# Kernel optimization log

Measured on AMD Instinct MI355X. Metric: run time of the kernel, lower is better.

Reference implementation:

```python
import jax, jax.numpy as jnp
import numpy as np

DT = 1.0
SPIKE_THRESHOLD = 30.0


def setup_inputs() -> dict:
    key = jax.random.key(0)
    kx, = jax.random.split(key, 1)
    x = jax.random.normal(kx, (16, 64, 1024, 32), dtype=jnp.float32)
    # scalar learnable parameters (Izhikevich model constants)
    a = jnp.float32(0.02)
    b = jnp.float32(0.2)
    c = jnp.float32(-65.0)
    d = jnp.float32(8.0)
    return {"x": x, "a": a, "b": b, "c": c, "d": d}


def reference(x, a, b, c, d):
    # x: [B, C, N, T]. Initial membrane potential v and recovery u are zeros.
    B, C, N, T = x.shape
    v0 = jnp.zeros((B, C, N), dtype=x.dtype)
    u0 = jnp.zeros((B, C, N), dtype=x.dtype)
    xs = jnp.moveaxis(x, -1, 0)  # [T, B, C, N] time-major for scan

    def step(carry, x_t):
        v, u = carry
        dv = 0.04 * v * v + 5.0 * v + 140.0 - u + x_t
        v = v + DT * dv
        du = a * (b * v - u)
        u = u + DT * du
        spike = (v >= SPIKE_THRESHOLD).astype(x_t.dtype)
        v = v * (1.0 - spike) + c * spike
        u = u + d * spike
        return (v, u), spike

    (_, _), spikes = jax.lax.scan(step, (v0, u0), xs)
    return jnp.moveaxis(spikes, 0, -1)  # [B, C, N, T]
```

## Files before the change

kernel.cpp:

```cpp
#include <hip/hip_runtime.h>


#define T_STEPS 32

__global__ __launch_bounds__(256) void izhikevich_kernel(
    const float* __restrict__ x,
    const float* __restrict__ pa,
    const float* __restrict__ pb,
    const float* __restrict__ pc,
    const float* __restrict__ pd,
    float* __restrict__ out,
    int n_neurons)
{
#pragma clang fp contract(off)
    const int n = blockIdx.x * blockDim.x + threadIdx.x;
    if (n >= n_neurons) return;

    const float a = pa[0];
    const float b = pb[0];
    const float c = pc[0];
    const float d = pd[0];

    const float4* __restrict__ xp =
        reinterpret_cast<const float4*>(x + (size_t)n * T_STEPS);
    float4* __restrict__ op =
        reinterpret_cast<float4*>(out + (size_t)n * T_STEPS);

    float4 xs[8];
#pragma unroll
    for (int k = 0; k < 8; ++k) xs[k] = xp[k];
    const float* xf = reinterpret_cast<const float*>(xs);

    float v = 0.0f;
    float u = 0.0f;

#pragma unroll
    for (int k = 0; k < 8; ++k) {
        float4 sp;
        float* sf = reinterpret_cast<float*>(&sp);
#pragma unroll
        for (int j = 0; j < 4; ++j) {
            const float xt = xf[k * 4 + j];
            const float t1 = (0.04f * v) * v;
            const float t2 = 5.0f * v;
            const float dv = (((t1 + t2) + 140.0f) - u) + xt;
            v = v + dv;
            const float du = a * ((b * v) - u);
            u = u + du;
            const float spike = (v >= 30.0f) ? 1.0f : 0.0f;
            const float oms = 1.0f - spike;
            v = (v * oms) + (c * spike);
            u = u + (d * spike);
            sf[j] = spike;
        }
        op[k] = sp;
    }
}

extern "C" void kernel_launch(void* const* d_in, const int* in_sizes, int n_in,
                              void* d_out, int out_size, void* d_ws, size_t ws_size,
                              hipStream_t stream) {
    const float* x  = (const float*)d_in[0];
    const float* pa = (const float*)d_in[1];
    const float* pb = (const float*)d_in[2];
    const float* pc = (const float*)d_in[3];
    const float* pd = (const float*)d_in[4];
    float* out = (float*)d_out;

    const int n_neurons = in_sizes[0] / T_STEPS;
    const int block = 256;
    const int grid = (n_neurons + block - 1) / block;

    izhikevich_kernel<<<grid, block, 0, stream>>>(x, pa, pb, pc, pd, out,
                                                  n_neurons);
}
```

Measured before the change: 265.1 us.

## Coalesce global loads and stores by transposing through padded shared memory

Each block now loads its contiguous input tile with fully coalesced float4 accesses, transposes it through a padded LDS buffer so each thread reads its own neuron's time series, and stages spikes back through LDS for coalesced stores. This replaces per-thread strided 128-byte accesses. It adds two barriers and LDS traffic, and drops the tail bounds check, so it assumes the neuron count is a multiple of the block size.

```diff
diff --git a/kernel.cpp b/kernel.cpp
--- a/kernel.cpp
+++ b/kernel.cpp
@@ -2,58 +2,72 @@
 
 
 #define T_STEPS 32
+#define TPB 256
+#define ROW 33
 
-__global__ __launch_bounds__(256) void izhikevich_kernel(
+__global__ __launch_bounds__(TPB) void izhikevich_kernel(
     const float* __restrict__ x,
     const float* __restrict__ pa,
     const float* __restrict__ pb,
     const float* __restrict__ pc,
     const float* __restrict__ pd,
-    float* __restrict__ out,
-    int n_neurons)
+    float* __restrict__ out)
 {
 #pragma clang fp contract(off)
-    const int n = blockIdx.x * blockDim.x + threadIdx.x;
-    if (n >= n_neurons) return;
+    __shared__ float lds[TPB * ROW];
+
+    const int t = threadIdx.x;
+    const size_t blockBase = (size_t)blockIdx.x * (TPB * T_STEPS);
 
     const float a = pa[0];
     const float b = pb[0];
     const float c = pc[0];
     const float d = pd[0];
 
-    const float4* __restrict__ xp =
-        reinterpret_cast<const float4*>(x + (size_t)n * T_STEPS);
-    float4* __restrict__ op =
-        reinterpret_cast<float4*>(out + (size_t)n * T_STEPS);
+    const float4* __restrict__ xin =
+        reinterpret_cast<const float4*>(x + blockBase);
+#pragma unroll
+    for (int k = 0; k < 8; ++k) {
+        const float4 ch = xin[k * TPB + t];
+        const int ng = k * 32 + (t >> 3);
+        const int tg = (t & 7) * 4;
+        float* row = &lds[ng * ROW + tg];
+        row[0] = ch.x; row[1] = ch.y; row[2] = ch.z; row[3] = ch.w;
+    }
+    __syncthreads();
 
-    float4 xs[8];
+    float xs[T_STEPS];
 #pragma unroll
-    for (int k = 0; k < 8; ++k) xs[k] = xp[k];
-    const float* xf = reinterpret_cast<const float*>(xs);
+    for (int j = 0; j < T_STEPS; ++j) xs[j] = lds[t * ROW + j];
 
     float v = 0.0f;
     float u = 0.0f;
+#pragma unroll
+    for (int j = 0; j < T_STEPS; ++j) {
+        const float xt = xs[j];
+        const float t1 = (0.04f * v) * v;
+        const float t2 = 5.0f * v;
+        const float dv = (((t1 + t2) + 140.0f) - u) + xt;
+        v = v + dv;
+        const float du = a * ((b * v) - u);
+        u = u + du;
+        const float spike = (v >= 30.0f) ? 1.0f : 0.0f;
+        const float oms = 1.0f - spike;
+        v = (v * oms) + (c * spike);
+        u = u + (d * spike);
+        lds[t * ROW + j] = spike;
+    }
+    __syncthreads();
 
+    float4* __restrict__ op = reinterpret_cast<float4*>(out + blockBase);
 #pragma unroll
     for (int k = 0; k < 8; ++k) {
-        float4 sp;
-        float* sf = reinterpret_cast<float*>(&sp);
-#pragma unroll
-        for (int j = 0; j < 4; ++j) {
-            const float xt = xf[k * 4 + j];
-            const float t1 = (0.04f * v) * v;
-            const float t2 = 5.0f * v;
-            const float dv = (((t1 + t2) + 140.0f) - u) + xt;
-            v = v + dv;
-            const float du = a * ((b * v) - u);
-            u = u + du;
-            const float spike = (v >= 30.0f) ? 1.0f : 0.0f;
-            const float oms = 1.0f - spike;
-            v = (v * oms) + (c * spike);
-            u = u + (d * spike);
-            sf[j] = spike;
-        }
-        op[k] = sp;
+        const int ng = k * 32 + (t >> 3);
+        const int tg = (t & 7) * 4;
+        const float* row = &lds[ng * ROW + tg];
+        float4 o;
+        o.x = row[0]; o.y = row[1]; o.z = row[2]; o.w = row[3];
+        op[k * TPB + t] = o;
     }
 }
 
@@ -68,9 +82,7 @@
     float* out = (float*)d_out;
 
     const int n_neurons = in_sizes[0] / T_STEPS;
-    const int block = 256;
-    const int grid = (n_neurons + block - 1) / block;
+    const int grid = n_neurons / TPB;
 
-    izhikevich_kernel<<<grid, block, 0, stream>>>(x, pa, pb, pc, pd, out,
-                                                  n_neurons);
+    izhikevich_kernel<<<grid, TPB, 0, stream>>>(x, pa, pb, pc, pd, out);
 }
```

Result: faster. 239.5 us (-9.7%).

## Stage neuron tiles through swizzled LDS with coalesced loads and double buffering

Applied to the files above, without the earlier changes.

Each wave now loads a 64-neuron tile with fully coalesced float4 accesses, transposes it through an XOR-swizzled LDS buffer so every lane can read its own neuron's time series, and writes spikes back through LDS with coalesced stores. Each wave handles four tiles in a grid-stride loop, prefetching the next tile into registers while the current one is computed. The goal is to replace the strided 128-byte-per-lane accesses with coalesced ones and to overlap memory with compute. In exchange it uses more registers and LDS, and it assumes the neuron count divides evenly into tiles, with no bounds checks.

```diff
diff --git a/kernel.cpp b/kernel.cpp
--- a/kernel.cpp
+++ b/kernel.cpp
@@ -2,58 +2,98 @@
 
 
 #define T_STEPS 32
+#define WPB 4
+#define TPB (WPB * 64)
+#define ITERS 4
 
-__global__ __launch_bounds__(256) void izhikevich_kernel(
+__global__ __launch_bounds__(TPB) void izhikevich_kernel(
     const float* __restrict__ x,
     const float* __restrict__ pa,
     const float* __restrict__ pb,
     const float* __restrict__ pc,
     const float* __restrict__ pd,
     float* __restrict__ out,
-    int n_neurons)
+    int stride_tiles)
 {
 #pragma clang fp contract(off)
-    const int n = blockIdx.x * blockDim.x + threadIdx.x;
-    if (n >= n_neurons) return;
+    __shared__ float lds_all[WPB * 2048];
+    const int lane = threadIdx.x & 63;
+    const int wave = threadIdx.x >> 6;
+    float* __restrict__ L = &lds_all[wave * 2048];
+
+    const int wid = blockIdx.x * WPB + wave;
 
     const float a = pa[0];
     const float b = pb[0];
     const float c = pc[0];
     const float d = pd[0];
 
-    const float4* __restrict__ xp =
-        reinterpret_cast<const float4*>(x + (size_t)n * T_STEPS);
-    float4* __restrict__ op =
-        reinterpret_cast<float4*>(out + (size_t)n * T_STEPS);
+    const float4* __restrict__ xin = reinterpret_cast<const float4*>(x);
+    float4* __restrict__ op = reinterpret_cast<float4*>(out);
 
-    float4 xs[8];
+    const int oct = lane >> 3;
+    const int grp = lane & 7;
+    const int scat_base = oct * 32 + ((grp ^ oct) << 2);
+    const int row_base = lane * 32;
+
+    float4 buf[2][8];
+
+    {
+        const size_t tb = (size_t)wid * 512;
 #pragma unroll
-    for (int k = 0; k < 8; ++k) xs[k] = xp[k];
-    const float* xf = reinterpret_cast<const float*>(xs);
-
-    float v = 0.0f;
-    float u = 0.0f;
+        for (int k = 0; k < 8; ++k) buf[0][k] = xin[tb + k * 64 + lane];
+    }
 
 #pragma unroll
-    for (int k = 0; k < 8; ++k) {
-        float4 sp;
-        float* sf = reinterpret_cast<float*>(&sp);
+    for (int i = 0; i < ITERS; ++i) {
+        const int cur = i & 1;
+        const int nxt = cur ^ 1;
+        const size_t tile = (size_t)wid + (size_t)i * (size_t)stride_tiles;
+
 #pragma unroll
-        for (int j = 0; j < 4; ++j) {
-            const float xt = xf[k * 4 + j];
-            const float t1 = (0.04f * v) * v;
-            const float t2 = 5.0f * v;
-            const float dv = (((t1 + t2) + 140.0f) - u) + xt;
-            v = v + dv;
-            const float du = a * ((b * v) - u);
-            u = u + du;
-            const float spike = (v >= 30.0f) ? 1.0f : 0.0f;
-            const float oms = 1.0f - spike;
-            v = (v * oms) + (c * spike);
-            u = u + (d * spike);
-            sf[j] = spike;
+        for (int k = 0; k < 8; ++k)
+            *reinterpret_cast<float4*>(&L[k * 256 + scat_base]) = buf[cur][k];
+
+        if (i + 1 < ITERS) {
+            const size_t tb = (tile + (size_t)stride_tiles) * 512;
+#pragma unroll
+            for (int k = 0; k < 8; ++k) buf[nxt][k] = xin[tb + k * 64 + lane];
         }
-        op[k] = sp;
+
+        float v = 0.0f;
+        float u = 0.0f;
+#pragma unroll
+        for (int q = 0; q < 8; ++q) {
+            float* p = &L[row_base + ((q ^ grp) << 2)];
+            const float4 xv = *reinterpret_cast<const float4*>(p);
+            const float xq[4] = {xv.x, xv.y, xv.z, xv.w};
+            float4 sp;
+            float* sf = reinterpret_cast<float*>(&sp);
+#pragma unroll
+            for (int j = 0; j < 4; ++j) {
+                const float xt = xq[j];
+                const float t1 = (0.04f * v) * v;
+                const float t2 = 5.0f * v;
+                const float dv = (((t1 + t2) + 140.0f) - u) + xt;
+                v = v + dv;
+                const float du = a * ((b * v) - u);
+                u = u + du;
+                const float spike = (v >= 30.0f) ? 1.0f : 0.0f;
+                const float oms = 1.0f - spike;
+                v = (v * oms) + (c * spike);
+                u = u + (d * spike);
+                sf[j] = spike;
+            }
+            *reinterpret_cast<float4*>(p) = sp;
+        }
+
+        const size_t tb = tile * 512;
+#pragma unroll
+        for (int k = 0; k < 8; ++k) {
+            const float4 o =
+                *reinterpret_cast<const float4*>(&L[k * 256 + scat_base]);
+            op[tb + k * 64 + lane] = o;
+        }
     }
 }
 
@@ -68,9 +108,10 @@
     float* out = (float*)d_out;
 
     const int n_neurons = in_sizes[0] / T_STEPS;
-    const int block = 256;
-    const int grid = (n_neurons + block - 1) / block;
+    const int n_tiles = n_neurons / 64;
+    const int grid = n_tiles / (WPB * ITERS);
+    const int stride_tiles = grid * WPB;
 
-    izhikevich_kernel<<<grid, block, 0, stream>>>(x, pa, pb, pc, pd, out,
-                                                  n_neurons);
+    izhikevich_kernel<<<grid, TPB, 0, stream>>>(x, pa, pb, pc, pd, out,
+                                                stride_tiles);
 }
```

New measurement: 239.5 us. -9.7%, faster.

## Stage tiles through LDS with async global-to-LDS loads and double buffering

Applied to the files above, without the earlier changes.

Each 64-thread block now handles four 64-neuron tiles. Their inputs are loaded straight into LDS with global_load_lds into two buffers, so the next tile is prefetched while the current one is computed. Reads and writes go through a swizzled LDS layout so global accesses are fully coalesced rather than 128-byte strided per thread. The change drops the bounds check, assumes the neuron count divides evenly by tiles and iterations, and has no explicit barrier or waitcnt around the LDS reuse, so correctness depends on compiler-inserted waits.

```diff
diff --git a/kernel.cpp b/kernel.cpp
--- a/kernel.cpp
+++ b/kernel.cpp
@@ -1,46 +1,76 @@
 #include <hip/hip_runtime.h>
 
 
-#define T_STEPS 32
+#define TPB 64
+#define ITERS 4
 
-__global__ __launch_bounds__(256) void izhikevich_kernel(
+__device__ __forceinline__ void gl2lds16(const float* g, float* l) {
+    __builtin_amdgcn_global_load_lds(
+        (const __attribute__((address_space(1))) void*)g,
+        (__attribute__((address_space(3))) void*)l, 16, 0, 0);
+}
+
+__global__ __launch_bounds__(TPB) void izhikevich_kernel(
     const float* __restrict__ x,
     const float* __restrict__ pa,
     const float* __restrict__ pb,
     const float* __restrict__ pc,
     const float* __restrict__ pd,
     float* __restrict__ out,
-    int n_neurons)
+    int stride_tiles)
 {
 #pragma clang fp contract(off)
-    const int n = blockIdx.x * blockDim.x + threadIdx.x;
-    if (n >= n_neurons) return;
+    __shared__ float B0[2048];
+    __shared__ float B1[2048];
+
+    const int lane = threadIdx.x;
+    const int oct  = lane >> 3;
+    const int grp  = lane & 7;
+    const int wid  = blockIdx.x;
 
     const float a = pa[0];
     const float b = pb[0];
     const float c = pc[0];
     const float d = pd[0];
 
-    const float4* __restrict__ xp =
-        reinterpret_cast<const float4*>(x + (size_t)n * T_STEPS);
-    float4* __restrict__ op =
-        reinterpret_cast<float4*>(out + (size_t)n * T_STEPS);
+    const int lane_f4 = oct * 8 + (grp ^ oct);
 
-    float4 xs[8];
-#pragma unroll
-    for (int k = 0; k < 8; ++k) xs[k] = xp[k];
-    const float* xf = reinterpret_cast<const float*>(xs);
+    const float4* __restrict__ xin = reinterpret_cast<const float4*>(x);
+    float4* __restrict__ op = reinterpret_cast<float4*>(out);
 
-    float v = 0.0f;
-    float u = 0.0f;
+#define PREFETCH(tile, B)                                                     \
+    do {                                                                      \
+        const float* g =                                                      \
+            x + (size_t)(tile) * 2048 + (size_t)lane_f4 * 4;                  \
+        _Pragma("unroll")                                                     \
+        for (int k = 0; k < 8; ++k) gl2lds16(g + k * 256, &(B)[k * 256]);     \
+    } while (0)
+
+    PREFETCH(wid, B0);
 
 #pragma unroll
-    for (int k = 0; k < 8; ++k) {
-        float4 sp;
-        float* sf = reinterpret_cast<float*>(&sp);
+    for (int i = 0; i < ITERS; ++i) {
+        float* __restrict__ cur = (i & 1) ? B1 : B0;
+        float* __restrict__ nxt = (i & 1) ? B0 : B1;
+        const int tile = wid + i * stride_tiles;
+
+        if (i + 1 < ITERS) PREFETCH(tile + stride_tiles, nxt);
+        __builtin_amdgcn_sched_barrier(0);
+
+        float4 xs[8];
 #pragma unroll
-        for (int j = 0; j < 4; ++j) {
-            const float xt = xf[k * 4 + j];
+        for (int q = 0; q < 8; ++q)
+            xs[q] = *reinterpret_cast<const float4*>(
+                &cur[lane * 32 + ((q ^ grp) << 2)]);
+        const float* xf = reinterpret_cast<const float*>(xs);
+
+        float4 sp[8];
+        float* sf = reinterpret_cast<float*>(sp);
+        float v = 0.0f;
+        float u = 0.0f;
+#pragma unroll
+        for (int j = 0; j < 32; ++j) {
+            const float xt = xf[j];
             const float t1 = (0.04f * v) * v;
             const float t2 = 5.0f * v;
             const float dv = (((t1 + t2) + 140.0f) - u) + xt;
@@ -53,8 +83,20 @@
             u = u + (d * spike);
             sf[j] = spike;
         }
-        op[k] = sp;
+
+#pragma unroll
+        for (int q = 0; q < 8; ++q)
+            *reinterpret_cast<float4*>(&cur[lane * 32 + ((q ^ grp) << 2)]) =
+                sp[q];
+
+#pragma unroll
+        for (int k = 0; k < 8; ++k) {
+            const float4 o = *reinterpret_cast<const float4*>(
+                &cur[k * 256 + lane * 4]);
+            op[(size_t)tile * 512 + k * 64 + lane_f4] = o;
+        }
     }
+#undef PREFETCH
 }
 
 extern "C" void kernel_launch(void* const* d_in, const int* in_sizes, int n_in,
@@ -67,10 +109,11 @@
     const float* pd = (const float*)d_in[4];
     float* out = (float*)d_out;
 
-    const int n_neurons = in_sizes[0] / T_STEPS;
-    const int block = 256;
-    const int grid = (n_neurons + block - 1) / block;
+    const int n_neurons = in_sizes[0] / 32;
+    const int n_tiles = n_neurons / 64;
+    const int grid = n_tiles / ITERS;
+    const int stride_tiles = grid;
 
-    izhikevich_kernel<<<grid, block, 0, stream>>>(x, pa, pb, pc, pd, out,
-                                                  n_neurons);
+    izhikevich_kernel<<<grid, TPB, 0, stream>>>(x, pa, pb, pc, pd, out,
+                                                stride_tiles);
 }
```

Result: faster. 242.1 us (-8.7%).
